# Optimization experiments

Measured on AMD Instinct MI355X. Metric: run time of the kernel, lower is better.

## Reference

```python
import jax, jax.numpy as jnp
import numpy as np

N_NODES = 100000
N_EDGES = 1600000
D_IN = 256
D_OUT = 128


def setup_inputs() -> dict:
    key = jax.random.key(0)
    ks = jax.random.split(key, 7)
    h = jax.random.normal(ks[0], (N_NODES, D_IN), dtype=jnp.float32)
    src = jax.random.randint(ks[1], (N_EDGES,), 0, N_NODES, dtype=jnp.int32)
    dst = jax.random.randint(ks[2], (N_EDGES,), 0, N_NODES, dtype=jnp.int32)
    W = jax.random.normal(ks[3], (D_IN, D_OUT), dtype=jnp.float32) * (1.0 / np.sqrt(D_IN))
    b = jax.random.normal(ks[4], (D_OUT,), dtype=jnp.float32) * 0.01
    w_att = jax.random.normal(ks[5], (2 * D_OUT, 1), dtype=jnp.float32) * (1.0 / np.sqrt(2 * D_OUT))
    b_att = jax.random.normal(ks[6], (1,), dtype=jnp.float32) * 0.01
    return {"h": h, "src": src, "dst": dst, "W": W, "b": b, "w_att": w_att, "b_att": b_att}


def reference(h, src, dst, W, b, w_att, b_att):
    # node projection: graph.ndata['h'] = self.linear(h)
    hp = h @ W + b  # [N, D_OUT]
    n = hp.shape[0]
    d = hp.shape[1]
    # edge attention: leaky_relu(att_linear(cat[h_src, h_dst]))
    # cat([hs, hd]) @ w_att == hs @ w_att[:d] + hd @ w_att[d:]  (avoids [E, 2d] concat)
    wa_s = w_att[:d, 0]  # [D_OUT]
    wa_d = w_att[d:, 0]  # [D_OUT]
    e = hp[src] @ wa_s + hp[dst] @ wa_d + b_att[0]  # [E]
    e = jax.nn.leaky_relu(e)  # default negative_slope 0.01 matches F.leaky_relu
    # segment softmax over each destination node's incoming edges
    emax = jax.ops.segment_max(e, dst, num_segments=n)  # [N]
    ex = jnp.exp(e - emax[dst])  # [E]
    denom = jax.ops.segment_sum(ex, dst, num_segments=n)  # [N]
    # weighted scatter-sum of src features: sum_e alpha_e * h_src_e
    num = jax.ops.segment_sum(ex[:, None] * hp[src], dst, num_segments=n)  # [N, D_OUT]
    out = num / jnp.where(denom > 0, denom, 1.0)[:, None]  # zero-in-degree nodes -> 0
    return out
```

## Files before the change

### kernel.cpp

```cpp
#include <hip/hip_runtime.h>
#include <hip/hip_bf16.h>

#define D_IN 256
#define D_OUT 128
#define BNODES 64
#define BCAP 1536
#define EPB 8192
#define MAXNB 1600

typedef __attribute__((ext_vector_type(8))) short bf16x8;
typedef __attribute__((ext_vector_type(4))) float f32x4;

__device__ __forceinline__ unsigned short f2bf(float f) {
    unsigned u = __float_as_uint(f);
    unsigned r = ((u >> 16) & 1u) + 0x7FFFu;
    return (unsigned short)((u + r) >> 16);
}
__device__ __forceinline__ unsigned pk2(float a, float b) {
    return (unsigned)f2bf(a) | ((unsigned)f2bf(b) << 16);
}
__device__ __forceinline__ bf16x8 pack8(float4 a, float4 b) {
    union { uint4 u; bf16x8 v; } r;
    r.u.x = pk2(a.x, a.y); r.u.y = pk2(a.z, a.w);
    r.u.z = pk2(b.x, b.y); r.u.w = pk2(b.z, b.w);
    return r.v;
}
__device__ __forceinline__ void gload_lds16(const void* g, void* l) {
    __builtin_amdgcn_global_load_lds(
        (const __attribute__((address_space(1))) void*)g,
        (__attribute__((address_space(3))) void*)l, 16, 0, 0);
}

__global__ __launch_bounds__(256) void init_bcursor_kernel(int* __restrict__ bcursor, int nb)
{
    int i = blockIdx.x * 256 + threadIdx.x;
    if (i < nb) bcursor[i] = i * BCAP;
}

__global__ __launch_bounds__(256) void prep_kernel(
    const float* __restrict__ W, unsigned short* __restrict__ WbT)
{
    int idx = blockIdx.x * 256 + threadIdx.x;
    int k = idx >> 7;
    int c = idx & 127;
    WbT[(size_t)c * 256 + k] = f2bf(W[idx]);
}

__global__ __launch_bounds__(256, 3) void gemm_mfma_kernel(
    const float* __restrict__ h, const unsigned short* __restrict__ WbT,
    const float* __restrict__ b, const float* __restrict__ w_att,
    unsigned short* __restrict__ hpb,
    float* __restrict__ alpha_s, float* __restrict__ alpha_d, int n)
{
    __shared__ char bT[32768];
    const int t = threadIdx.x;
    const int wv = t >> 6, lane = t & 63;
    const int fr = lane & 15, fq = lane >> 4;
    const int r0 = blockIdx.x * 128 + wv * 32;
    const int swz = (fr & 7) << 4;

    const int scol = wv * 32 + (lane >> 4) - ((lane >> 4) & 3) * 0;
    auto stage = [&](int hh) {
        #pragma unroll
        for (int j = 0; j < 8; ++j) {
            int col0 = wv * 32 + j * 4;
            int col = col0 + (lane >> 4);
            int seg = lane & 15;
            const char* src = (const char*)WbT + col * 512 + hh * 256
                            + ((seg * 16) ^ ((col & 7) << 4));
            gload_lds16(src, bT + col0 * 256);
        }
    };
    (void)scol;

    stage(0);

    const float* arow[2];
    #pragma unroll
    for (int m = 0; m < 2; ++m) {
        int rg = r0 + m * 16 + fr;
        if (rg >= n) rg = n - 1;
        arow[m] = h + (size_t)rg * D_IN + fq * 8;
    }

    f32x4 acc[2][8];
    #pragma unroll
    for (int m = 0; m < 2; ++m)
        #pragma unroll
        for (int nn = 0; nn < 8; ++nn) acc[m][nn] = (f32x4){0.f, 0.f, 0.f, 0.f};

    float4 bufA[2][2][2];
    #pragma unroll
    for (int m = 0; m < 2; ++m) {
        const float4* ap = (const float4*)arow[m];
        bufA[0][m][0] = ap[0]; bufA[0][m][1] = ap[1];
    }
    __syncthreads();

    #pragma unroll
    for (int kk = 0; kk < 8; ++kk) {
        if (kk == 4) {
            __syncthreads();
            stage(1);
            __syncthreads();
        }
        const int cur = kk & 1, nxt = cur ^ 1;
        if (kk < 7) {
            #pragma unroll
            for (int m = 0; m < 2; ++m) {
                const float4* ap = (const float4*)(arow[m] + (kk + 1) * 32);
                bufA[nxt][m][0] = ap[0]; bufA[nxt][m][1] = ap[1];
            }
        }
        bf16x8 af[2];
        #pragma unroll
        for (int m = 0; m < 2; ++m)
            af[m] = pack8(bufA[cur][m][0], bufA[cur][m][1]);

        const int x = (kk & 3) * 64 + fq * 16;
        #pragma unroll
        for (int nn = 0; nn < 8; ++nn) {
            bf16x8 bfr = *(const bf16x8*)(bT + (nn * 16 + fr) * 256 + (x ^ swz));
            acc[0][nn] = __builtin_amdgcn_mfma_f32_16x16x32_bf16(af[0], bfr, acc[0][nn], 0, 0, 0);
            acc[1][nn] = __builtin_amdgcn_mfma_f32_16x16x32_bf16(af[1], bfr, acc[1][nn], 0, 0, 0);
        }
    }

    float bcol[8], was[8], wad[8];
    #pragma unroll
    for (int nn = 0; nn < 8; ++nn) {
        int j = nn * 16 + fr;
        bcol[nn] = b[j]; was[nn] = w_att[j]; wad[nn] = w_att[D_OUT + j];
    }
    #pragma unroll
    for (int m = 0; m < 2; ++m) {
        #pragma unroll
        for (int reg = 0; reg < 4; ++reg) {
            const int grow = r0 + m * 16 + fq * 4 + reg;
            const bool ok = grow < n;
            float ps = 0.f, pd = 0.f;
            #pragma unroll
            for (int nn = 0; nn < 8; ++nn) {
                float vv = acc[m][nn][reg] + bcol[nn];
                ps += vv * was[nn];
                pd += vv * wad[nn];
                if (ok) hpb[(size_t)grow * D_OUT + nn * 16 + fr] = f2bf(vv);
            }
            #pragma unroll
            for (int o = 1; o < 16; o <<= 1) {
                ps += __shfl_xor(ps, o);
                pd += __shfl_xor(pd, o);
            }
            if (fr == 0 && ok) { alpha_s[grow] = ps; alpha_d[grow] = pd; }
        }
    }
}

__global__ __launch_bounds__(1024) void bucket_scatter_kernel(
    const int* __restrict__ src, const int* __restrict__ dst,
    const float* __restrict__ alpha_s, const float* __restrict__ alpha_d,
    const float* __restrict__ b_att, int* __restrict__ bcursor,
    int2* __restrict__ ebuf, int ne, int nb)
{
    __shared__ int lhist[MAXNB];
    __shared__ int gbase[MAXNB];
    __shared__ int lcur[MAXNB];
    const int t = threadIdx.x;
    for (int i = t; i < nb; i += 1024) { lhist[i] = 0; lcur[i] = 0; }
    __syncthreads();
    const int base = blockIdx.x * EPB;
    #pragma unroll
    for (int j = 0; j < EPB / 1024; ++j) {
        int idx = base + j * 1024 + t;
        if (idx < ne) atomicAdd(&lhist[dst[idx] >> 6], 1);
    }
    __syncthreads();
    for (int i = t; i < nb; i += 1024) {
        int c = lhist[i];
        gbase[i] = c ? atomicAdd(&bcursor[i], c) : 0;
    }
    __syncthreads();
    const float ba = b_att[0];
    #pragma unroll
    for (int j = 0; j < EPB / 1024; ++j) {
        int idx = base + j * 1024 + t;
        if (idx < ne) {
            int s = src[idx], d = dst[idx];
            float ev = alpha_s[s] + alpha_d[d] + ba;
            ev = (ev >= 0.f) ? ev : 0.01f * ev;
            int bkt = d >> 6;
            int pos = gbase[bkt] + atomicAdd(&lcur[bkt], 1);
            if (pos < (bkt + 1) * BCAP)
                ebuf[pos] = make_int2(s | ((d & 63) << 17), __float_as_int(ev));
        }
    }
}

#define ACCUM8(uvar, wvar)                                     \
    acc[0] += (wvar) * __uint_as_float((uvar).x << 16);        \
    acc[1] += (wvar) * __uint_as_float((uvar).x & 0xFFFF0000u);\
    acc[2] += (wvar) * __uint_as_float((uvar).y << 16);        \
    acc[3] += (wvar) * __uint_as_float((uvar).y & 0xFFFF0000u);\
    acc[4] += (wvar) * __uint_as_float((uvar).z << 16);        \
    acc[5] += (wvar) * __uint_as_float((uvar).z & 0xFFFF0000u);\
    acc[6] += (wvar) * __uint_as_float((uvar).w << 16);        \
    acc[7] += (wvar) * __uint_as_float((uvar).w & 0xFFFF0000u);

__global__ __launch_bounds__(256) void aggregate_kernel(
    const unsigned short* __restrict__ hpb, const int2* __restrict__ ebuf,
    const int* __restrict__ bcursor, float* __restrict__ out, int n)
{
    __shared__ int2 srec[BCAP];
    __shared__ int lhist[BNODES], lstart[BNODES], lcur[BNODES];
    const int t = threadIdx.x;
    const int bk = blockIdx.x;
    const int node0 = bk << 6;
    const int base = bk * BCAP;
    int cnt = bcursor[bk] - base;
    cnt = min(cnt, BCAP);

    if (t < BNODES) lhist[t] = 0;
    __syncthreads();
    for (int i = t; i < cnt; i += 256)
        atomicAdd(&lhist[(ebuf[base + i].x >> 17) & 63], 1);
    __syncthreads();
    if (t < BNODES) {
        int c0 = lhist[t];
        int incl = c0;
        #pragma unroll
        for (int o = 1; o < 64; o <<= 1) {
            int v = __shfl_up(incl, o);
            if (t >= o) incl += v;
        }
        lstart[t] = incl - c0;
        lcur[t]   = incl - c0;
    }
    __syncthreads();
    for (int i = t; i < cnt; i += 256) {
        int2 r = ebuf[base + i];
        int pos = atomicAdd(&lcur[(r.x >> 17) & 63], 1);
        srec[pos] = r;
    }
    __syncthreads();

    const int wv = t >> 6, lane = t & 63;
    const int q = lane >> 4, dlane = lane & 15;
    const uint4* hp4 = (const uint4*)hpb;

    #pragma unroll
    for (int p = 0; p < 4; ++p) {
        const int nd = p * 16 + wv * 4 + q;
        const int gnode = node0 + nd;
        const int off = lstart[nd], c = lhist[nd];

        float m = -INFINITY;
        for (int i = dlane; i < c; i += 16)
            m = fmaxf(m, __int_as_float(srec[off + i].y));
        #pragma unroll
        for (int o = 8; o; o >>= 1) m = fmaxf(m, __shfl_xor(m, o));

        float acc[8] = {0.f,0.f,0.f,0.f,0.f,0.f,0.f,0.f};
        float denom = 0.f;

        for (int t0 = 0; t0 < c; t0 += 4) {
            const int cm1 = c - 1;
            int2 r0 = srec[off + min(t0 + 0, cm1)];
            int2 r1 = srec[off + min(t0 + 1, cm1)];
            int2 r2 = srec[off + min(t0 + 2, cm1)];
            int2 r3 = srec[off + min(t0 + 3, cm1)];
            float w0 = __expf(__int_as_float(r0.y) - m);
            float w1 = (t0 + 1 < c) ? __expf(__int_as_float(r1.y) - m) : 0.f;
            float w2 = (t0 + 2 < c) ? __expf(__int_as_float(r2.y) - m) : 0.f;
            float w3 = (t0 + 3 < c) ? __expf(__int_as_float(r3.y) - m) : 0.f;
            uint4 u0 = hp4[(size_t)(r0.x & 0x1FFFF) * 16 + dlane];
            uint4 u1 = hp4[(size_t)(r1.x & 0x1FFFF) * 16 + dlane];
            uint4 u2 = hp4[(size_t)(r2.x & 0x1FFFF) * 16 + dlane];
            uint4 u3 = hp4[(size_t)(r3.x & 0x1FFFF) * 16 + dlane];
            ACCUM8(u0, w0) denom += w0;
            ACCUM8(u1, w1) denom += w1;
            ACCUM8(u2, w2) denom += w2;
            ACCUM8(u3, w3) denom += w3;
        }

        if (gnode < n) {
            float inv = (c > 0) ? 1.f / denom : 0.f;
            float4 o0 = { acc[0]*inv, acc[1]*inv, acc[2]*inv, acc[3]*inv };
            float4 o1 = { acc[4]*inv, acc[5]*inv, acc[6]*inv, acc[7]*inv };
            float4* op = (float4*)(out + (size_t)gnode * D_OUT) + 2 * dlane;
            op[0] = o0;
            op[1] = o1;
        }
    }
}

extern "C" void kernel_launch(void* const* d_in, const int* in_sizes, int n_in,
                              void* d_out, int out_size, void* d_ws, size_t ws_size,
                              hipStream_t stream)
{
    const float* h     = (const float*)d_in[0];
    const int*   src   = (const int*)  d_in[1];
    const int*   dst   = (const int*)  d_in[2];
    const float* W     = (const float*)d_in[3];
    const float* b     = (const float*)d_in[4];
    const float* w_att = (const float*)d_in[5];
    const float* b_att = (const float*)d_in[6];
    float* out = (float*)d_out;

    const int n  = in_sizes[0] / D_IN;
    const int ne = in_sizes[1];
    const int nb = (n + BNODES - 1) / BNODES;

    unsigned short* hpb = (unsigned short*)d_ws;
    float* alpha_s = (float*)d_ws + (size_t)n * 64;
    float* alpha_d = alpha_s + n;
    int2*  ebuf    = (int2*)(alpha_d + n);
    int*   bcursor = (int*)(ebuf + (size_t)nb * BCAP);
    unsigned short* WbT = (unsigned short*)(bcursor + nb);

    init_bcursor_kernel<<<(nb + 255) / 256, 256, 0, stream>>>(bcursor, nb);
    prep_kernel<<<128, 256, 0, stream>>>(W, WbT);
    gemm_mfma_kernel<<<(n + 127) / 128, 256, 0, stream>>>(
        h, WbT, b, w_att, hpb, alpha_s, alpha_d, n);
    bucket_scatter_kernel<<<(ne + EPB - 1) / EPB, 1024, 0, stream>>>(
        src, dst, alpha_s, alpha_d, b_att, bcursor, ebuf, ne, nb);
    aggregate_kernel<<<nb, 256, 0, stream>>>(hpb, ebuf, bcursor, out, n);
}
```

Before: 139.5 us.

## Stage full W tile once in 512-thread GEMM, precompute softmax weights in aggregate

The GEMM kernel now uses 512 threads with a 64KB LDS tile that holds all of W^T. It is staged once up front, which removes the mid-loop restage and its extra barriers. Each wave handles one 32-row strip. The aggregate kernel also moves to 512 threads, so 8 waves each handle 2 nodes. A parallel pass over all edges in the bucket now computes the exp weights and denominators (via LDS atomics) and writes the weights back into srec, so the inner gather loop no longer computes exp. The larger LDS footprint and the early return of idle waves after the barrier may reduce occupancy.

```diff
diff --git a/kernel.cpp b/kernel.cpp
--- a/kernel.cpp
+++ b/kernel.cpp
@@ -10,6 +10,7 @@
 
 typedef __attribute__((ext_vector_type(8))) short bf16x8;
 typedef __attribute__((ext_vector_type(4))) float f32x4;
+typedef __attribute__((ext_vector_type(2))) float f32x2;
 
 __device__ __forceinline__ unsigned short f2bf(float f) {
     unsigned u = __float_as_uint(f);
@@ -46,34 +47,32 @@
     WbT[(size_t)c * 256 + k] = f2bf(W[idx]);
 }
 
-__global__ __launch_bounds__(256, 3) void gemm_mfma_kernel(
+__global__ __launch_bounds__(512, 4) void gemm_mfma_kernel(
     const float* __restrict__ h, const unsigned short* __restrict__ WbT,
     const float* __restrict__ b, const float* __restrict__ w_att,
     unsigned short* __restrict__ hpb,
-    float* __restrict__ alpha_s, float* __restrict__ alpha_d, int n)
-{
-    __shared__ char bT[32768];
+    float* __restrict__ alpha_s, float* __restrict__ alpha_d,
+    int n, int nstrips)
+{
+    __shared__ char bT[65536];
     const int t = threadIdx.x;
     const int wv = t >> 6, lane = t & 63;
     const int fr = lane & 15, fq = lane >> 4;
-    const int r0 = blockIdx.x * 128 + wv * 32;
     const int swz = (fr & 7) << 4;
 
-    const int scol = wv * 32 + (lane >> 4) - ((lane >> 4) & 3) * 0;
-    auto stage = [&](int hh) {
-        #pragma unroll
-        for (int j = 0; j < 8; ++j) {
-            int col0 = wv * 32 + j * 4;
-            int col = col0 + (lane >> 4);
-            int seg = lane & 15;
-            const char* src = (const char*)WbT + col * 512 + hh * 256
-                            + ((seg * 16) ^ ((col & 7) << 4));
-            gload_lds16(src, bT + col0 * 256);
-        }
-    };
-    (void)scol;
-
-    stage(0);
+    #pragma unroll
+    for (int j = 0; j < 8; ++j) {
+        int col0 = wv * 16 + j * 2;
+        int col  = col0 + (lane >> 5);
+        int seg  = lane & 31;
+        const char* src = (const char*)WbT + col * 512 + ((seg * 16) ^ ((col & 7) << 4));
+        gload_lds16(src, bT + col0 * 512);
+    }
+    __syncthreads();
+
+    const int strip = blockIdx.x * 8 + wv;
+    if (strip >= nstrips) return;
+    const int r0 = strip * 32;
 
     const float* arow[2];
     #pragma unroll
@@ -95,15 +94,9 @@
         const float4* ap = (const float4*)arow[m];
         bufA[0][m][0] = ap[0]; bufA[0][m][1] = ap[1];
     }
-    __syncthreads();
 
     #pragma unroll
     for (int kk = 0; kk < 8; ++kk) {
-        if (kk == 4) {
-            __syncthreads();
-            stage(1);
-            __syncthreads();
-        }
         const int cur = kk & 1, nxt = cur ^ 1;
         if (kk < 7) {
             #pragma unroll
@@ -117,10 +110,10 @@
         for (int m = 0; m < 2; ++m)
             af[m] = pack8(bufA[cur][m][0], bufA[cur][m][1]);
 
-        const int x = (kk & 3) * 64 + fq * 16;
+        const int x = kk * 64 + fq * 16;
         #pragma unroll
         for (int nn = 0; nn < 8; ++nn) {
-            bf16x8 bfr = *(const bf16x8*)(bT + (nn * 16 + fr) * 256 + (x ^ swz));
+            bf16x8 bfr = *(const bf16x8*)(bT + (nn * 16 + fr) * 512 + (x ^ swz));
             acc[0][nn] = __builtin_amdgcn_mfma_f32_16x16x32_bf16(af[0], bfr, acc[0][nn], 0, 0, 0);
             acc[1][nn] = __builtin_amdgcn_mfma_f32_16x16x32_bf16(af[1], bfr, acc[1][nn], 0, 0, 0);
         }
@@ -196,22 +189,24 @@
     }
 }
 
-#define ACCUM8(uvar, wvar)                                     \
-    acc[0] += (wvar) * __uint_as_float((uvar).x << 16);        \
-    acc[1] += (wvar) * __uint_as_float((uvar).x & 0xFFFF0000u);\
-    acc[2] += (wvar) * __uint_as_float((uvar).y << 16);        \
-    acc[3] += (wvar) * __uint_as_float((uvar).y & 0xFFFF0000u);\
-    acc[4] += (wvar) * __uint_as_float((uvar).z << 16);        \
-    acc[5] += (wvar) * __uint_as_float((uvar).z & 0xFFFF0000u);\
-    acc[6] += (wvar) * __uint_as_float((uvar).w << 16);        \
-    acc[7] += (wvar) * __uint_as_float((uvar).w & 0xFFFF0000u);
-
-__global__ __launch_bounds__(256) void aggregate_kernel(
+__device__ __forceinline__ void acc8(f32x2* acc2, uint4 uv, float w) {
+    acc2[0].x += w * __uint_as_float(uv.x << 16);
+    acc2[0].y += w * __uint_as_float(uv.x & 0xFFFF0000u);
+    acc2[1].x += w * __uint_as_float(uv.y << 16);
+    acc2[1].y += w * __uint_as_float(uv.y & 0xFFFF0000u);
+    acc2[2].x += w * __uint_as_float(uv.z << 16);
+    acc2[2].y += w * __uint_as_float(uv.z & 0xFFFF0000u);
+    acc2[3].x += w * __uint_as_float(uv.w << 16);
+    acc2[3].y += w * __uint_as_float(uv.w & 0xFFFF0000u);
+}
+
+__global__ __launch_bounds__(512) void aggregate_kernel(
     const unsigned short* __restrict__ hpb, const int2* __restrict__ ebuf,
     const int* __restrict__ bcursor, float* __restrict__ out, int n)
 {
     __shared__ int2 srec[BCAP];
     __shared__ int lhist[BNODES], lstart[BNODES], lcur[BNODES];
+    __shared__ float lmax[BNODES], lden[BNODES];
     const int t = threadIdx.x;
     const int bk = blockIdx.x;
     const int node0 = bk << 6;
@@ -219,9 +214,9 @@
     int cnt = bcursor[bk] - base;
     cnt = min(cnt, BCAP);
 
-    if (t < BNODES) lhist[t] = 0;
-    __syncthreads();
-    for (int i = t; i < cnt; i += 256)
+    if (t < BNODES) { lhist[t] = 0; lden[t] = 0.f; }
+    __syncthreads();
+    for (int i = t; i < cnt; i += 512)
         atomicAdd(&lhist[(ebuf[base + i].x >> 17) & 63], 1);
     __syncthreads();
     if (t < BNODES) {
@@ -236,7 +231,7 @@
         lcur[t]   = incl - c0;
     }
     __syncthreads();
-    for (int i = t; i < cnt; i += 256) {
+    for (int i = t; i < cnt; i += 512) {
         int2 r = ebuf[base + i];
         int pos = atomicAdd(&lcur[(r.x >> 17) & 63], 1);
         srec[pos] = r;
@@ -248,19 +243,36 @@
     const uint4* hp4 = (const uint4*)hpb;
 
     #pragma unroll
-    for (int p = 0; p < 4; ++p) {
-        const int nd = p * 16 + wv * 4 + q;
-        const int gnode = node0 + nd;
+    for (int p = 0; p < 2; ++p) {
+        const int nd = p * 32 + wv * 4 + q;
         const int off = lstart[nd], c = lhist[nd];
-
         float m = -INFINITY;
         for (int i = dlane; i < c; i += 16)
             m = fmaxf(m, __int_as_float(srec[off + i].y));
         #pragma unroll
         for (int o = 8; o; o >>= 1) m = fmaxf(m, __shfl_xor(m, o));
-
-        float acc[8] = {0.f,0.f,0.f,0.f,0.f,0.f,0.f,0.f};
-        float denom = 0.f;
+        if (dlane == 0) lmax[nd] = m;
+    }
+    __syncthreads();
+
+    for (int i = t; i < cnt; i += 512) {
+        int2 r = srec[i];
+        int nd = (r.x >> 17) & 63;
+        float w = __expf(__int_as_float(r.y) - lmax[nd]);
+        srec[i].y = __float_as_int(w);
+        atomicAdd(&lden[nd], w);
+    }
+    __syncthreads();
+
+    #pragma unroll
+    for (int p = 0; p < 2; ++p) {
+        const int nd = p * 32 + wv * 4 + q;
+        const int gnode = node0 + nd;
+        const int off = lstart[nd], c = lhist[nd];
+
+        f32x2 acc2[4];
+        #pragma unroll
+        for (int k = 0; k < 4; ++k) acc2[k] = (f32x2){0.f, 0.f};
 
         for (int t0 = 0; t0 < c; t0 += 4) {
             const int cm1 = c - 1;
@@ -268,24 +280,24 @@
             int2 r1 = srec[off + min(t0 + 1, cm1)];
             int2 r2 = srec[off + min(t0 + 2, cm1)];
             int2 r3 = srec[off + min(t0 + 3, cm1)];
-            float w0 = __expf(__int_as_float(r0.y) - m);
-            float w1 = (t0 + 1 < c) ? __expf(__int_as_float(r1.y) - m) : 0.f;
-            float w2 = (t0 + 2 < c) ? __expf(__int_as_float(r2.y) - m) : 0.f;
-            float w3 = (t0 + 3 < c) ? __expf(__int_as_float(r3.y) - m) : 0.f;
+            float w0 = __int_as_float(r0.y);
+            float w1 = (t0 + 1 < c) ? __int_as_float(r1.y) : 0.f;
+            float w2 = (t0 + 2 < c) ? __int_as_float(r2.y) : 0.f;
+            float w3 = (t0 + 3 < c) ? __int_as_float(r3.y) : 0.f;
             uint4 u0 = hp4[(size_t)(r0.x & 0x1FFFF) * 16 + dlane];
             uint4 u1 = hp4[(size_t)(r1.x & 0x1FFFF) * 16 + dlane];
             uint4 u2 = hp4[(size_t)(r2.x & 0x1FFFF) * 16 + dlane];
             uint4 u3 = hp4[(size_t)(r3.x & 0x1FFFF) * 16 + dlane];
-            ACCUM8(u0, w0) denom += w0;
-            ACCUM8(u1, w1) denom += w1;
-            ACCUM8(u2, w2) denom += w2;
-            ACCUM8(u3, w3) denom += w3;
+            acc8(acc2, u0, w0);
+            acc8(acc2, u1, w1);
+            acc8(acc2, u2, w2);
+            acc8(acc2, u3, w3);
         }
 
         if (gnode < n) {
-            float inv = (c > 0) ? 1.f / denom : 0.f;
-            float4 o0 = { acc[0]*inv, acc[1]*inv, acc[2]*inv, acc[3]*inv };
-            float4 o1 = { acc[4]*inv, acc[5]*inv, acc[6]*inv, acc[7]*inv };
+            float inv = (c > 0) ? 1.f / lden[nd] : 0.f;
+            float4 o0 = { acc2[0].x*inv, acc2[0].y*inv, acc2[1].x*inv, acc2[1].y*inv };
+            float4 o1 = { acc2[2].x*inv, acc2[2].y*inv, acc2[3].x*inv, acc2[3].y*inv };
             float4* op = (float4*)(out + (size_t)gnode * D_OUT) + 2 * dlane;
             op[0] = o0;
             op[1] = o1;
@@ -309,6 +321,7 @@
     const int n  = in_sizes[0] / D_IN;
     const int ne = in_sizes[1];
     const int nb = (n + BNODES - 1) / BNODES;
+    const int nstrips = (n + 31) / 32;
 
     unsigned short* hpb = (unsigned short*)d_ws;
     float* alpha_s = (float*)d_ws + (size_t)n * 64;
@@ -319,9 +332,9 @@
 
     init_bcursor_kernel<<<(nb + 255) / 256, 256, 0, stream>>>(bcursor, nb);
     prep_kernel<<<128, 256, 0, stream>>>(W, WbT);
-    gemm_mfma_kernel<<<(n + 127) / 128, 256, 0, stream>>>(
-        h, WbT, b, w_att, hpb, alpha_s, alpha_d, n);
+    gemm_mfma_kernel<<<(nstrips + 7) / 8, 512, 0, stream>>>(
+        h, WbT, b, w_att, hpb, alpha_s, alpha_d, n, nstrips);
     bucket_scatter_kernel<<<(ne + EPB - 1) / EPB, 1024, 0, stream>>>(
         src, dst, alpha_s, alpha_d, b_att, bcursor, ebuf, ne, nb);
-    aggregate_kernel<<<nb, 256, 0, stream>>>(hpb, ebuf, bcursor, out, n);
-}
+    aggregate_kernel<<<nb, 512, 0, stream>>>(hpb, ebuf, bcursor, out, n);
+}
```

Result: no change. 138.9 us (-0.4%).
